# Performance work log

Measured on AMD Instinct MI355X. Metric: run time of the kernel, lower is better.

Reference implementation:

```python
import jax, jax.numpy as jnp
import numpy as np

N_NODES = 100000
N_EDGES = 300000
D_NODE_IN = 128
D_EDGE_IN = 4
LATENT = 256
HIDDEN = 256
STEPS = 6
D_OUT = 128
LN_EPS = 1e-5


def _mlp(x, w1, b1, w2, b2):
    # hk.nets.MLP([HIDDEN, out], activation=swish): act on hidden, none on output
    return jax.nn.swish(x @ w1 + b1) @ w2 + b2


def _ln(x, scale, offset):
    m = jnp.mean(x, axis=-1, keepdims=True)
    c = x - m
    v = jnp.mean(c * c, axis=-1, keepdims=True)
    return c * jax.lax.rsqrt(v + LN_EPS) * scale + offset


def setup_inputs():
    key = jax.random.key(0)
    ks = iter(jax.random.split(key, 40))

    def w(shape):
        fan_in = shape[-2]
        return (jax.random.normal(next(ks), shape, jnp.float32) / np.sqrt(fan_in).astype(np.float32))

    inp = {}
    inp['node_features'] = jax.random.normal(next(ks), (N_NODES, D_NODE_IN), jnp.float32)
    inp['edge_features'] = jax.random.normal(next(ks), (N_EDGES, D_EDGE_IN), jnp.float32)
    inp['senders'] = jax.random.randint(next(ks), (N_EDGES,), 0, N_NODES, jnp.int32)
    inp['receivers'] = jax.random.randint(next(ks), (N_EDGES,), 0, N_NODES, jnp.int32)
    # encoder (embed) MLPs + LayerNorm
    inp['enc_node_w1'] = w((D_NODE_IN, HIDDEN)); inp['enc_node_b1'] = jnp.zeros((HIDDEN,), jnp.float32)
    inp['enc_node_w2'] = w((HIDDEN, LATENT)); inp['enc_node_b2'] = jnp.zeros((LATENT,), jnp.float32)
    inp['enc_node_ln_s'] = jnp.ones((LATENT,), jnp.float32); inp['enc_node_ln_o'] = jnp.zeros((LATENT,), jnp.float32)
    inp['enc_edge_w1'] = w((D_EDGE_IN, HIDDEN)); inp['enc_edge_b1'] = jnp.zeros((HIDDEN,), jnp.float32)
    inp['enc_edge_w2'] = w((HIDDEN, LATENT)); inp['enc_edge_b2'] = jnp.zeros((LATENT,), jnp.float32)
    inp['enc_edge_ln_s'] = jnp.ones((LATENT,), jnp.float32); inp['enc_edge_ln_o'] = jnp.zeros((LATENT,), jnp.float32)
    # processor: STEPS unshared InteractionNetwork layers, weights stacked on axis 0
    inp['pe_w1'] = w((STEPS, 3 * LATENT, HIDDEN)); inp['pe_b1'] = jnp.zeros((STEPS, HIDDEN), jnp.float32)
    inp['pe_w2'] = w((STEPS, HIDDEN, LATENT)); inp['pe_b2'] = jnp.zeros((STEPS, LATENT), jnp.float32)
    inp['pe_ln_s'] = jnp.ones((STEPS, LATENT), jnp.float32); inp['pe_ln_o'] = jnp.zeros((STEPS, LATENT), jnp.float32)
    inp['pn_w1'] = w((STEPS, 2 * LATENT, HIDDEN)); inp['pn_b1'] = jnp.zeros((STEPS, HIDDEN), jnp.float32)
    inp['pn_w2'] = w((STEPS, HIDDEN, LATENT)); inp['pn_b2'] = jnp.zeros((STEPS, LATENT), jnp.float32)
    inp['pn_ln_s'] = jnp.ones((STEPS, LATENT), jnp.float32); inp['pn_ln_o'] = jnp.zeros((STEPS, LATENT), jnp.float32)
    # decoder (output) MLP, no LayerNorm
    inp['dec_w1'] = w((LATENT, HIDDEN)); inp['dec_b1'] = jnp.zeros((HIDDEN,), jnp.float32)
    inp['dec_w2'] = w((HIDDEN, D_OUT)); inp['dec_b2'] = jnp.zeros((D_OUT,), jnp.float32)
    return inp


def reference(node_features, edge_features, senders, receivers,
              enc_node_w1, enc_node_b1, enc_node_w2, enc_node_b2, enc_node_ln_s, enc_node_ln_o,
              enc_edge_w1, enc_edge_b1, enc_edge_w2, enc_edge_b2, enc_edge_ln_s, enc_edge_ln_o,
              pe_w1, pe_b1, pe_w2, pe_b2, pe_ln_s, pe_ln_o,
              pn_w1, pn_b1, pn_w2, pn_b2, pn_ln_s, pn_ln_o,
              dec_w1, dec_b1, dec_w2, dec_b2):
    # Embed nodes and edges into latent space (MLP + LayerNorm).
    node = _ln(_mlp(node_features, enc_node_w1, enc_node_b1, enc_node_w2, enc_node_b2), enc_node_ln_s, enc_node_ln_o)
    edge = _ln(_mlp(edge_features, enc_edge_w1, enc_edge_b1, enc_edge_w2, enc_edge_b2), enc_edge_ln_s, enc_edge_ln_o)

    n_nodes = node.shape[0]

    def step(carry, p):
        node, edge = carry
        ew1, eb1, ew2, eb2, els, elo, nw1, nb1, nw2, nb2, nls, nlo = p
        # edge update: MLP(concat[edge, sender_node, receiver_node]) + residual
        msg_in = jnp.concatenate([edge, node[senders], node[receivers]], axis=-1)  # [E, 3*LATENT]
        edge = edge + _ln(_mlp(msg_in, ew1, eb1, ew2, eb2), els, elo)
        # aggregate messages to receiver nodes
        agg = jax.ops.segment_sum(edge, receivers, num_segments=n_nodes)  # [N, LATENT]
        # node update: MLP(concat[node, agg]) + residual
        node = node + _ln(_mlp(jnp.concatenate([node, agg], axis=-1), nw1, nb1, nw2, nb2), nls, nlo)
        return (node, edge), None

    (node, edge), _ = jax.lax.scan(
        step, (node, edge),
        (pe_w1, pe_b1, pe_w2, pe_b2, pe_ln_s, pe_ln_o,
         pn_w1, pn_b1, pn_w2, pn_b2, pn_ln_s, pn_ln_o))

    # decoder: plain MLP (no LayerNorm) on nodes only (node_output_size given).
    return _mlp(node, dec_w1, dec_b1, dec_w2, dec_b2)  # [N, D_OUT]
```

## Files before the change

### kernel.cpp

```cpp
#include <hip/hip_runtime.h>
#include <hip/hip_bf16.h>


#define NN 100000
#define NE 300000

typedef __attribute__((ext_vector_type(8))) short bf16x8;
typedef __attribute__((ext_vector_type(8))) unsigned short u16x8;
typedef __attribute__((ext_vector_type(4))) float f32x4;

typedef const __attribute__((address_space(1))) void cg1_t;
typedef __attribute__((address_space(3))) void l3_t;
static __device__ __forceinline__ void gld_lds16(const void* g, void* l) {
  __builtin_amdgcn_global_load_lds((cg1_t*)g, (l3_t*)l, 16, 0, 0);
}

static __device__ __forceinline__ unsigned short f2bf(float f) {
  union { float f; unsigned u; } v; v.f = f;
  unsigned r = v.u + 0x7FFFu + ((v.u >> 16) & 1u);
  unsigned short h = (unsigned short)(r >> 16);
  if ((h & 0x7F80u) == 0x7F80u) h = 0;
  return h;
}
static __device__ __forceinline__ float bf2f(unsigned short h) {
  union { unsigned u; float f; } v; v.u = ((unsigned)h) << 16;
  return v.f;
}

struct KArgs {
  const float* Xf;
  unsigned short* nodeB;
  unsigned short* edgeB;
  const unsigned short* aggB;
  const int* snd;
  const int* rcv;
  const unsigned short* W1p;
  const unsigned short* W2p;
  const float* b1;
  const float* b2;
  const float* lns;
  const float* lno;
  float* outF;
  int M;
};

__global__ void pack_w(const float* __restrict__ src,
                       unsigned short* __restrict__ dst,
                       int Ksrc, int Kpad, int N) {
  src += (size_t)blockIdx.y * Ksrc * N;
  dst += (size_t)blockIdx.y * Kpad * N;
  int fi = blockIdx.x;
  int nfr = N >> 4;
  int nb = fi % nfr, kb = fi / nfr;
  int t = threadIdx.x;
  int lane = t >> 3, j = t & 7;
  int k = kb * 32 + ((lane >> 4) * 8) + j;
  int col = nb * 16 + (lane & 15);
  unsigned short v = (k < Ksrc) ? f2bf(src[(size_t)k * N + col]) : (unsigned short)0;
  dst[(size_t)fi * 512 + t] = v;
}

__global__ void zero_ws(uint4* __restrict__ p, int n16) {
  uint4 z = {0u, 0u, 0u, 0u};
  for (int i = blockIdx.x * blockDim.x + threadIdx.x; i < n16;
       i += gridDim.x * blockDim.x)
    p[i] = z;
}

__global__ void hist_k(const int* __restrict__ rcv, int* __restrict__ cnt) {
  int e = blockIdx.x * blockDim.x + threadIdx.x;
  if (e < NE) {
    int r = rcv[e]; r = r < 0 ? 0 : (r > NN - 1 ? NN - 1 : r);
    atomicAdd(&cnt[r], 1);
  }
}

__global__ __launch_bounds__(1024)
void scan_k(const int* __restrict__ cnt, int* __restrict__ off) {
  __shared__ int wsum[16];
  __shared__ int carry_s, tot_s;
  int t = threadIdx.x, lane = t & 63, w = t >> 6;
  if (t == 0) carry_s = 0;
  __syncthreads();
  for (int base = 0; base < NN; base += 1024) {
    int i = base + t;
    int v = (i < NN) ? cnt[i] : 0;
    int incl = v;
    #pragma unroll
    for (int d = 1; d < 64; d <<= 1) {
      int u = __shfl_up(incl, d);
      if (lane >= d) incl += u;
    }
    if (lane == 63) wsum[w] = incl;
    int c0 = carry_s;
    __syncthreads();
    if (t < 16) {
      int s = wsum[t];
      int isc = s;
      #pragma unroll
      for (int d = 1; d < 16; d <<= 1) {
        int u = __shfl_up(isc, d);
        if (t >= d) isc += u;
      }
      wsum[t] = isc - s;
    }
    __syncthreads();
    int excl = c0 + wsum[w] + incl - v;
    if (i < NN) off[i] = excl;
    if (t == 1023) tot_s = wsum[15] + incl;
    __syncthreads();
    if (t == 0) carry_s += tot_s;
    __syncthreads();
  }
  if (t == 0) off[NN] = carry_s;
}

__global__ void fill_k(const int* __restrict__ rcv, const int* __restrict__ off,
                       int* __restrict__ cnt2, int* __restrict__ eidx) {
  int e = blockIdx.x * blockDim.x + threadIdx.x;
  if (e < NE) {
    int r = rcv[e]; r = r < 0 ? 0 : (r > NN - 1 ? NN - 1 : r);
    int p = off[r] + atomicAdd(&cnt2[r], 1);
    if (p >= 0 && p < NE) eidx[p] = e;
  }
}

__global__ __launch_bounds__(256)
void agg_k(const unsigned short* __restrict__ edge, const int* __restrict__ off,
           const int* __restrict__ eidx, unsigned short* __restrict__ agg) {
  int t = threadIdx.x;
  int n0 = blockIdx.x * 8;
  #pragma unroll 1
  for (int u = 0; u < 8; ++u) {
    int n = n0 + u;
    if (n >= NN) return;
    int s = off[n], e = off[n + 1];
    if (s < 0) s = 0;
    if (e > NE) e = NE;
    float acc = 0.f;
    for (int i = s; i < e; ++i) {
      int eid = eidx[i];
      eid = eid < 0 ? 0 : (eid > NE - 1 ? NE - 1 : eid);
      acc += bf2f(edge[(size_t)eid * 256 + t]);
    }
    agg[(size_t)n * 256 + t] = f2bf(acc);
  }
}

template<int PHASE>
__global__ __launch_bounds__(512)
void gnn_kernel(KArgs A) {
  constexpr int K1  = PHASE==0?128 : PHASE==1?64 : PHASE==2?768 : PHASE==3?512 : 256;
  constexpr int NS1 = K1 / 64;
  constexpr int N2  = (PHASE==4) ? 128 : 256;
  constexpr int NF2 = N2 / 128;

  __shared__ __align__(16) char smem[50688];
  auto Ht  = (unsigned short (*)[264])(smem + 16384);
  int*   lidx = (int*)(smem + 50176);
  float* ps    = (float*)smem;
  float* ps2   = (float*)(smem + 2048);
  float* rs_mu = (float*)(smem + 4096);
  float* rs_rs = (float*)(smem + 4352);

  const int tid  = threadIdx.x;
  const int wid  = tid >> 6;
  const int lane = tid & 63;
  const int r0   = blockIdx.x * 64;
  const int M    = A.M;

  if constexpr (PHASE == 2) {
    if (tid < 64) {
      int e = r0 + tid; if (e > M - 1) e = M - 1;
      int v = A.snd[e]; v = v < 0 ? 0 : (v > NN - 1 ? NN - 1 : v);
      lidx[tid] = v;
    } else if (tid < 128) {
      int e = r0 + tid - 64; if (e > M - 1) e = M - 1;
      int v = A.rcv[e]; v = v < 0 ? 0 : (v > NN - 1 ? NN - 1 : v);
      lidx[tid] = v;
    }
  }
  __syncthreads();

  auto stage = [&](int ks, int b) {
    int r = tid >> 3;
    int c = (tid & 7) ^ (r & 7);
    int row = r0 + r; if (row > M - 1) row = M - 1;
    if constexpr (PHASE == 0) {
      const float* s = A.Xf + (size_t)row * 128 + ks * 64 + c * 8;
      float4 f0 = *(const float4*)s;
      float4 f1 = *(const float4*)(s + 4);
      u16x8 w;
      w[0]=f2bf(f0.x); w[1]=f2bf(f0.y); w[2]=f2bf(f0.z); w[3]=f2bf(f0.w);
      w[4]=f2bf(f1.x); w[5]=f2bf(f1.y); w[6]=f2bf(f1.z); w[7]=f2bf(f1.w);
      *(u16x8*)(smem + b * 8192 + r * 128 + (tid & 7) * 16) = w;
    } else if constexpr (PHASE == 1) {
      u16x8 w = (u16x8){0,0,0,0,0,0,0,0};
      if (c == 0) {
        float4 f = *(const float4*)(A.Xf + (size_t)row * 4);
        w[0]=f2bf(f.x); w[1]=f2bf(f.y); w[2]=f2bf(f.z); w[3]=f2bf(f.w);
      }
      *(u16x8*)(smem + b * 8192 + r * 128 + (tid & 7) * 16) = w;
    } else {
      const unsigned short* src;
      if constexpr (PHASE == 2) {
        if (ks < 4) {
          src = A.edgeB + (size_t)row * 256 + ks * 64 + c * 8;
        } else {
          int nidx = (ks < 8) ? lidx[r] : lidx[64 + r];
          int koff = (ks < 8) ? (ks - 4) * 64 : (ks - 8) * 64;
          src = A.nodeB + (size_t)nidx * 256 + koff + c * 8;
        }
      } else if constexpr (PHASE == 3) {
        src = (ks < 4) ? A.nodeB + (size_t)row * 256 + ks * 64 + c * 8
                       : A.aggB  + (size_t)row * 256 + (ks - 4) * 64 + c * 8;
      } else {
        src = A.nodeB + (size_t)row * 256 + ks * 64 + c * 8;
      }
      gld_lds16(src, smem + b * 8192 + wid * 1024);
    }
  };

  const int mrow  = lane & 15;
  const int rbase = (lane >> 4) * 4;
  const int swz   = mrow & 7;

  f32x4 zero4 = {0.f, 0.f, 0.f, 0.f};
  f32x4 acc1[4][2];
  #pragma unroll
  for (int m = 0; m < 4; ++m) { acc1[m][0] = zero4; acc1[m][1] = zero4; }

  stage(0, 0);
  __syncthreads();
  for (int ks = 0; ks < NS1; ++ks) {
    if (ks + 1 < NS1) stage(ks + 1, (ks + 1) & 1);
    const char* buf = smem + (ks & 1) * 8192;
    #pragma unroll
    for (int kk = 0; kk < 2; ++kk) {
      int ch = (kk * 4 + (lane >> 4)) ^ swz;
      const char* p0 = buf + (mrow) * 128 + ch * 16;
      bf16x8 a0 = *(const bf16x8*)(p0);
      bf16x8 a1 = *(const bf16x8*)(p0 + 16 * 128);
      bf16x8 a2 = *(const bf16x8*)(p0 + 32 * 128);
      bf16x8 a3 = *(const bf16x8*)(p0 + 48 * 128);
      bf16x8 b0 = *(const bf16x8*)(A.W1p + ((size_t)((2 * ks + kk) * 16 + wid * 2 + 0) * 64 + lane) * 8);
      bf16x8 b1 = *(const bf16x8*)(A.W1p + ((size_t)((2 * ks + kk) * 16 + wid * 2 + 1) * 64 + lane) * 8);
      acc1[0][0] = __builtin_amdgcn_mfma_f32_16x16x32_bf16(a0, b0, acc1[0][0], 0, 0, 0);
      acc1[0][1] = __builtin_amdgcn_mfma_f32_16x16x32_bf16(a0, b1, acc1[0][1], 0, 0, 0);
      acc1[1][0] = __builtin_amdgcn_mfma_f32_16x16x32_bf16(a1, b0, acc1[1][0], 0, 0, 0);
      acc1[1][1] = __builtin_amdgcn_mfma_f32_16x16x32_bf16(a1, b1, acc1[1][1], 0, 0, 0);
      acc1[2][0] = __builtin_amdgcn_mfma_f32_16x16x32_bf16(a2, b0, acc1[2][0], 0, 0, 0);
      acc1[2][1] = __builtin_amdgcn_mfma_f32_16x16x32_bf16(a2, b1, acc1[2][1], 0, 0, 0);
      acc1[3][0] = __builtin_amdgcn_mfma_f32_16x16x32_bf16(a3, b0, acc1[3][0], 0, 0, 0);
      acc1[3][1] = __builtin_amdgcn_mfma_f32_16x16x32_bf16(a3, b1, acc1[3][1], 0, 0, 0);
    }
    __syncthreads();
  }

  #pragma unroll
  for (int nf = 0; nf < 2; ++nf) {
    int c = wid * 32 + nf * 16 + mrow;
    float bb = A.b1[c];
    #pragma unroll
    for (int m = 0; m < 4; ++m)
      #pragma unroll
      for (int j = 0; j < 4; ++j) {
        float x = acc1[m][nf][j] + bb;
        float h = x * (1.f / (1.f + __expf(-x)));
        Ht[m * 16 + rbase + j][c] = f2bf(h);
      }
  }
  __syncthreads();

  f32x4 acc2[4][NF2];
  #pragma unroll
  for (int m = 0; m < 4; ++m)
    #pragma unroll
    for (int nf = 0; nf < NF2; ++nf) acc2[m][nf] = zero4;

  const int kof = (lane >> 4) * 8;
  #pragma unroll
  for (int ks = 0; ks < 8; ++ks) {
    bf16x8 a[4], b[NF2];
    #pragma unroll
    for (int m = 0; m < 4; ++m)
      a[m] = *(const bf16x8*)&Ht[m * 16 + mrow][ks * 32 + kof];
    #pragma unroll
    for (int nf = 0; nf < NF2; ++nf)
      b[nf] = *(const bf16x8*)(A.W2p + ((size_t)(ks * (N2 / 16) + wid * NF2 + nf) * 64 + lane) * 8);
    #pragma unroll
    for (int m = 0; m < 4; ++m)
      #pragma unroll
      for (int nf = 0; nf < NF2; ++nf)
        acc2[m][nf] = __builtin_amdgcn_mfma_f32_16x16x32_bf16(a[m], b[nf], acc2[m][nf], 0, 0, 0);
  }

  if constexpr (PHASE == 4) {
    int c = wid * 16 + mrow;
    float bb = A.b2[c];
    #pragma unroll
    for (int m = 0; m < 4; ++m)
      #pragma unroll
      for (int j = 0; j < 4; ++j) {
        int rg = r0 + m * 16 + rbase + j;
        if (rg < M) A.outF[(size_t)rg * 128 + c] = acc2[m][0][j] + bb;
      }
  } else {
    const int cc0 = wid * 32 + mrow;
    const int cc1 = cc0 + 16;
    const float bb0 = A.b2[cc0];
    const float bb1 = A.b2[cc1];
    #pragma unroll
    for (int m = 0; m < 4; ++m)
      #pragma unroll
      for (int j = 0; j < 4; ++j) {
        acc2[m][0][j] += bb0;
        acc2[m][1][j] += bb1;
        float t  = acc2[m][0][j] + acc2[m][1][j];
        float t2 = acc2[m][0][j] * acc2[m][0][j] + acc2[m][1][j] * acc2[m][1][j];
        #pragma unroll
        for (int mk = 1; mk < 16; mk <<= 1) {
          t  += __shfl_xor(t, mk);
          t2 += __shfl_xor(t2, mk);
        }
        if (mrow == 0) {
          int row = m * 16 + rbase + j;
          ps [wid * 64 + row] = t;
          ps2[wid * 64 + row] = t2;
        }
      }
    __syncthreads();
    if (tid < 64) {
      float s = 0.f, q = 0.f;
      #pragma unroll
      for (int w = 0; w < 8; ++w) { s += ps[w * 64 + tid]; q += ps2[w * 64 + tid]; }
      float mu = s * (1.0f / 256.0f);
      float va = fmaxf(q * (1.0f / 256.0f) - mu * mu, 0.f);
      rs_mu[tid] = mu;
      rs_rs[tid] = rsqrtf(va + 1e-5f);
    }
    __syncthreads();
    const float ls0 = A.lns[cc0], lo0 = A.lno[cc0];
    const float ls1 = A.lns[cc1], lo1 = A.lno[cc1];
    #pragma unroll
    for (int m = 0; m < 4; ++m)
      #pragma unroll
      for (int j = 0; j < 4; ++j) {
        int row = m * 16 + rbase + j;
        int rg = r0 + row;
        if (rg >= M) continue;
        float mu = rs_mu[row], rstd = rs_rs[row];
        float y0 = (acc2[m][0][j] - mu) * rstd * ls0 + lo0;
        float y1 = (acc2[m][1][j] - mu) * rstd * ls1 + lo1;
        size_t base = (size_t)rg * 256;
        if constexpr (PHASE == 0) {
          A.nodeB[base + cc0] = f2bf(y0);
          A.nodeB[base + cc1] = f2bf(y1);
        } else if constexpr (PHASE == 1) {
          A.edgeB[base + cc0] = f2bf(y0);
          A.edgeB[base + cc1] = f2bf(y1);
        } else if constexpr (PHASE == 2) {
          A.edgeB[base + cc0] = f2bf(bf2f(A.edgeB[base + cc0]) + y0);
          A.edgeB[base + cc1] = f2bf(bf2f(A.edgeB[base + cc1]) + y1);
        } else {
          A.nodeB[base + cc0] = f2bf(bf2f(A.nodeB[base + cc0]) + y0);
          A.nodeB[base + cc1] = f2bf(bf2f(A.nodeB[base + cc1]) + y1);
        }
      }
  }
}

extern "C" void kernel_launch(void* const* d_in, const int* in_sizes, int n_in,
                              void* d_out, int out_size, void* d_ws, size_t ws_size,
                              hipStream_t stream) {
  (void)in_sizes; (void)n_in; (void)out_size; (void)ws_size;
  const float* x_node = (const float*)d_in[0];
  const float* x_edge = (const float*)d_in[1];
  const int* snd = (const int*)d_in[2];
  const int* rcv = (const int*)d_in[3];
  const float* en_w1 = (const float*)d_in[4];
  const float* en_b1 = (const float*)d_in[5];
  const float* en_w2 = (const float*)d_in[6];
  const float* en_b2 = (const float*)d_in[7];
  const float* en_ls = (const float*)d_in[8];
  const float* en_lo = (const float*)d_in[9];
  const float* ee_w1 = (const float*)d_in[10];
  const float* ee_b1 = (const float*)d_in[11];
  const float* ee_w2 = (const float*)d_in[12];
  const float* ee_b2 = (const float*)d_in[13];
  const float* ee_ls = (const float*)d_in[14];
  const float* ee_lo = (const float*)d_in[15];
  const float* pe_w1 = (const float*)d_in[16];
  const float* pe_b1 = (const float*)d_in[17];
  const float* pe_w2 = (const float*)d_in[18];
  const float* pe_b2 = (const float*)d_in[19];
  const float* pe_ls = (const float*)d_in[20];
  const float* pe_lo = (const float*)d_in[21];
  const float* pn_w1 = (const float*)d_in[22];
  const float* pn_b1 = (const float*)d_in[23];
  const float* pn_w2 = (const float*)d_in[24];
  const float* pn_b2 = (const float*)d_in[25];
  const float* pn_ls = (const float*)d_in[26];
  const float* pn_lo = (const float*)d_in[27];
  const float* dc_w1 = (const float*)d_in[28];
  const float* dc_b1 = (const float*)d_in[29];
  const float* dc_w2 = (const float*)d_in[30];
  const float* dc_b2 = (const float*)d_in[31];

  char* ws = (char*)d_ws;
  unsigned short* edgeB = (unsigned short*)(ws);
  unsigned short* nodeB = (unsigned short*)(ws + 153600000LL);
  unsigned short* aggB  = (unsigned short*)(ws + 204800000LL);

  unsigned short* wpck = (unsigned short*)d_out;
  size_t o = 0;
  auto nxt = [&](size_t n) { unsigned short* p = wpck + o; o += n; return p; };
  unsigned short* p_en_w1 = nxt(128 * 256);
  unsigned short* p_en_w2 = nxt(256 * 256);
  unsigned short* p_ee_w1 = nxt(64 * 256);
  unsigned short* p_ee_w2 = nxt(256 * 256);
  unsigned short* p_pe_w1 = nxt((size_t)6 * 768 * 256);
  unsigned short* p_pe_w2 = nxt((size_t)6 * 256 * 256);
  unsigned short* p_pn_w1 = nxt((size_t)6 * 512 * 256);
  unsigned short* p_pn_w2 = nxt((size_t)6 * 256 * 256);
  unsigned short* p_dc_w1 = nxt(256 * 256);
  unsigned short* p_dc_w2 = nxt(256 * 128);
  const size_t DC_BYTES = (256 * 256 + 256 * 128) * 2;

  char* outc = (char*)d_out;
  int* cnt  = (int*)(outc + 6062080);
  int* cnt2 = (int*)(outc + 6462080);
  int* off  = (int*)(outc + 6862080);
  int* eidx = (int*)(outc + 7262096);

  dim3 B(512);
  pack_w<<<dim3(4 * 16, 1), B, 0, stream>>>(en_w1, p_en_w1, 128, 128, 256);
  pack_w<<<dim3(8 * 16, 1), B, 0, stream>>>(en_w2, p_en_w2, 256, 256, 256);
  pack_w<<<dim3(2 * 16, 1), B, 0, stream>>>(ee_w1, p_ee_w1, 4, 64, 256);
  pack_w<<<dim3(8 * 16, 1), B, 0, stream>>>(ee_w2, p_ee_w2, 256, 256, 256);
  pack_w<<<dim3(24 * 16, 6), B, 0, stream>>>(pe_w1, p_pe_w1, 768, 768, 256);
  pack_w<<<dim3(8 * 16, 6), B, 0, stream>>>(pe_w2, p_pe_w2, 256, 256, 256);
  pack_w<<<dim3(16 * 16, 6), B, 0, stream>>>(pn_w1, p_pn_w1, 512, 512, 256);
  pack_w<<<dim3(8 * 16, 6), B, 0, stream>>>(pn_w2, p_pn_w2, 256, 256, 256);
  pack_w<<<dim3(8 * 16, 1), B, 0, stream>>>(dc_w1, p_dc_w1, 256, 256, 256);
  pack_w<<<dim3(8 * 8, 1), B, 0, stream>>>(dc_w2, p_dc_w2, 256, 256, 128);

  zero_ws<<<dim3(196), dim3(256), 0, stream>>>((uint4*)cnt, 800000 / 16);
  hist_k<<<dim3(1172), dim3(256), 0, stream>>>(rcv, cnt);
  scan_k<<<dim3(1), dim3(1024), 0, stream>>>(cnt, off);
  fill_k<<<dim3(1172), dim3(256), 0, stream>>>(rcv, off, cnt2, eidx);

  dim3 GN(1563), GE(4688);

  {
    KArgs a{}; a.Xf = x_node; a.W1p = p_en_w1; a.W2p = p_en_w2;
    a.b1 = en_b1; a.b2 = en_b2; a.lns = en_ls; a.lno = en_lo;
    a.nodeB = nodeB; a.M = NN;
    gnn_kernel<0><<<GN, B, 0, stream>>>(a);
  }
  {
    KArgs a{}; a.Xf = x_edge; a.W1p = p_ee_w1; a.W2p = p_ee_w2;
    a.b1 = ee_b1; a.b2 = ee_b2; a.lns = ee_ls; a.lno = ee_lo;
    a.edgeB = edgeB; a.M = NE;
    gnn_kernel<1><<<GE, B, 0, stream>>>(a);
  }
  for (int s = 0; s < 6; ++s) {
    {
      KArgs a{}; a.snd = snd; a.rcv = rcv;
      a.nodeB = nodeB; a.edgeB = edgeB;
      a.W1p = p_pe_w1 + (size_t)s * 768 * 256;
      a.W2p = p_pe_w2 + (size_t)s * 256 * 256;
      a.b1 = pe_b1 + s * 256; a.b2 = pe_b2 + s * 256;
      a.lns = pe_ls + s * 256; a.lno = pe_lo + s * 256;
      a.M = NE;
      gnn_kernel<2><<<GE, B, 0, stream>>>(a);
    }
    agg_k<<<dim3(12500), dim3(256), 0, stream>>>(edgeB, off, eidx, aggB);
    {
      KArgs a{}; a.nodeB = nodeB; a.aggB = aggB;
      a.W1p = p_pn_w1 + (size_t)s * 512 * 256;
      a.W2p = p_pn_w2 + (size_t)s * 256 * 256;
      a.b1 = pn_b1 + s * 256; a.b2 = pn_b2 + s * 256;
      a.lns = pn_ls + s * 256; a.lno = pn_lo + s * 256;
      a.M = NN;
      gnn_kernel<3><<<GN, B, 0, stream>>>(a);
    }
  }
  hipMemcpyAsync((void*)aggB, p_dc_w1, DC_BYTES, hipMemcpyDeviceToDevice, stream);
  {
    KArgs a{}; a.nodeB = nodeB;
    a.W1p = (const unsigned short*)aggB;
    a.W2p = (const unsigned short*)aggB + 256 * 256;
    a.b1 = dc_b1; a.b2 = dc_b2;
    a.outF = (float*)d_out; a.M = NN;
    gnn_kernel<4><<<GN, B, 0, stream>>>(a);
  }
}
```

Before: 3.191 ms.

## Deepen global-to-LDS prefetch and register-prefetch weights in GEMM1 K-loop

For the bf16 input phases, the first-GEMM K-loop now keeps two global_load_lds stages in flight. It waits with explicit vmcnt counts and raw s_barrier instead of __syncthreads, so the gather loads for the next tile overlap the current MFMAs. Weight fragments for the next K-step are loaded into registers one iteration ahead. Precomputed source pointers remove per-stage index arithmetic. The manual waitcnt handling is fragile: the register weight loads also count toward vmcnt, which may make the waits over-conservative or ordering-sensitive, and the prefetch raises register pressure.

```diff
diff --git a/kernel.cpp b/kernel.cpp
--- a/kernel.cpp
+++ b/kernel.cpp
@@ -182,45 +182,6 @@
   }
   __syncthreads();
 
-  auto stage = [&](int ks, int b) {
-    int r = tid >> 3;
-    int c = (tid & 7) ^ (r & 7);
-    int row = r0 + r; if (row > M - 1) row = M - 1;
-    if constexpr (PHASE == 0) {
-      const float* s = A.Xf + (size_t)row * 128 + ks * 64 + c * 8;
-      float4 f0 = *(const float4*)s;
-      float4 f1 = *(const float4*)(s + 4);
-      u16x8 w;
-      w[0]=f2bf(f0.x); w[1]=f2bf(f0.y); w[2]=f2bf(f0.z); w[3]=f2bf(f0.w);
-      w[4]=f2bf(f1.x); w[5]=f2bf(f1.y); w[6]=f2bf(f1.z); w[7]=f2bf(f1.w);
-      *(u16x8*)(smem + b * 8192 + r * 128 + (tid & 7) * 16) = w;
-    } else if constexpr (PHASE == 1) {
-      u16x8 w = (u16x8){0,0,0,0,0,0,0,0};
-      if (c == 0) {
-        float4 f = *(const float4*)(A.Xf + (size_t)row * 4);
-        w[0]=f2bf(f.x); w[1]=f2bf(f.y); w[2]=f2bf(f.z); w[3]=f2bf(f.w);
-      }
-      *(u16x8*)(smem + b * 8192 + r * 128 + (tid & 7) * 16) = w;
-    } else {
-      const unsigned short* src;
-      if constexpr (PHASE == 2) {
-        if (ks < 4) {
-          src = A.edgeB + (size_t)row * 256 + ks * 64 + c * 8;
-        } else {
-          int nidx = (ks < 8) ? lidx[r] : lidx[64 + r];
-          int koff = (ks < 8) ? (ks - 4) * 64 : (ks - 8) * 64;
-          src = A.nodeB + (size_t)nidx * 256 + koff + c * 8;
-        }
-      } else if constexpr (PHASE == 3) {
-        src = (ks < 4) ? A.nodeB + (size_t)row * 256 + ks * 64 + c * 8
-                       : A.aggB  + (size_t)row * 256 + (ks - 4) * 64 + c * 8;
-      } else {
-        src = A.nodeB + (size_t)row * 256 + ks * 64 + c * 8;
-      }
-      gld_lds16(src, smem + b * 8192 + wid * 1024);
-    }
-  };
-
   const int mrow  = lane & 15;
   const int rbase = (lane >> 4) * 4;
   const int swz   = mrow & 7;
@@ -230,31 +191,126 @@
   #pragma unroll
   for (int m = 0; m < 4; ++m) { acc1[m][0] = zero4; acc1[m][1] = zero4; }
 
-  stage(0, 0);
-  __syncthreads();
-  for (int ks = 0; ks < NS1; ++ks) {
-    if (ks + 1 < NS1) stage(ks + 1, (ks + 1) & 1);
-    const char* buf = smem + (ks & 1) * 8192;
-    #pragma unroll
-    for (int kk = 0; kk < 2; ++kk) {
-      int ch = (kk * 4 + (lane >> 4)) ^ swz;
-      const char* p0 = buf + (mrow) * 128 + ch * 16;
-      bf16x8 a0 = *(const bf16x8*)(p0);
-      bf16x8 a1 = *(const bf16x8*)(p0 + 16 * 128);
-      bf16x8 a2 = *(const bf16x8*)(p0 + 32 * 128);
-      bf16x8 a3 = *(const bf16x8*)(p0 + 48 * 128);
-      bf16x8 b0 = *(const bf16x8*)(A.W1p + ((size_t)((2 * ks + kk) * 16 + wid * 2 + 0) * 64 + lane) * 8);
-      bf16x8 b1 = *(const bf16x8*)(A.W1p + ((size_t)((2 * ks + kk) * 16 + wid * 2 + 1) * 64 + lane) * 8);
-      acc1[0][0] = __builtin_amdgcn_mfma_f32_16x16x32_bf16(a0, b0, acc1[0][0], 0, 0, 0);
-      acc1[0][1] = __builtin_amdgcn_mfma_f32_16x16x32_bf16(a0, b1, acc1[0][1], 0, 0, 0);
-      acc1[1][0] = __builtin_amdgcn_mfma_f32_16x16x32_bf16(a1, b0, acc1[1][0], 0, 0, 0);
-      acc1[1][1] = __builtin_amdgcn_mfma_f32_16x16x32_bf16(a1, b1, acc1[1][1], 0, 0, 0);
-      acc1[2][0] = __builtin_amdgcn_mfma_f32_16x16x32_bf16(a2, b0, acc1[2][0], 0, 0, 0);
-      acc1[2][1] = __builtin_amdgcn_mfma_f32_16x16x32_bf16(a2, b1, acc1[2][1], 0, 0, 0);
-      acc1[3][0] = __builtin_amdgcn_mfma_f32_16x16x32_bf16(a3, b0, acc1[3][0], 0, 0, 0);
-      acc1[3][1] = __builtin_amdgcn_mfma_f32_16x16x32_bf16(a3, b1, acc1[3][1], 0, 0, 0);
-    }
-    __syncthreads();
+  if constexpr (PHASE <= 1) {
+    auto stage = [&](int ks, int b) {
+      int r = tid >> 3;
+      int c = (tid & 7) ^ (r & 7);
+      int row = r0 + r; if (row > M - 1) row = M - 1;
+      u16x8 w;
+      if constexpr (PHASE == 0) {
+        const float* s = A.Xf + (size_t)row * 128 + ks * 64 + c * 8;
+        float4 f0 = *(const float4*)s;
+        float4 f1 = *(const float4*)(s + 4);
+        w[0]=f2bf(f0.x); w[1]=f2bf(f0.y); w[2]=f2bf(f0.z); w[3]=f2bf(f0.w);
+        w[4]=f2bf(f1.x); w[5]=f2bf(f1.y); w[6]=f2bf(f1.z); w[7]=f2bf(f1.w);
+      } else {
+        w = (u16x8){0,0,0,0,0,0,0,0};
+        if (c == 0) {
+          float4 f = *(const float4*)(A.Xf + (size_t)row * 4);
+          w[0]=f2bf(f.x); w[1]=f2bf(f.y); w[2]=f2bf(f.z); w[3]=f2bf(f.w);
+        }
+      }
+      *(u16x8*)(smem + b * 8192 + (tid >> 3) * 128 + (tid & 7) * 16) = w;
+    };
+    stage(0, 0);
+    __syncthreads();
+    #pragma unroll
+    for (int ks = 0; ks < NS1; ++ks) {
+      if (ks + 1 < NS1) stage(ks + 1, (ks + 1) & 1);
+      const char* buf = smem + (ks & 1) * 8192;
+      #pragma unroll
+      for (int kk = 0; kk < 2; ++kk) {
+        int ch = (kk * 4 + (lane >> 4)) ^ swz;
+        const char* p0 = buf + mrow * 128 + ch * 16;
+        bf16x8 a0 = *(const bf16x8*)(p0);
+        bf16x8 a1 = *(const bf16x8*)(p0 + 16 * 128);
+        bf16x8 a2 = *(const bf16x8*)(p0 + 32 * 128);
+        bf16x8 a3 = *(const bf16x8*)(p0 + 48 * 128);
+        const unsigned short* wb = A.W1p + ((size_t)((2 * ks + kk) * 16 + wid * 2) * 64 + lane) * 8;
+        bf16x8 b0 = *(const bf16x8*)(wb);
+        bf16x8 b1 = *(const bf16x8*)(wb + 512);
+        acc1[0][0] = __builtin_amdgcn_mfma_f32_16x16x32_bf16(a0, b0, acc1[0][0], 0, 0, 0);
+        acc1[0][1] = __builtin_amdgcn_mfma_f32_16x16x32_bf16(a0, b1, acc1[0][1], 0, 0, 0);
+        acc1[1][0] = __builtin_amdgcn_mfma_f32_16x16x32_bf16(a1, b0, acc1[1][0], 0, 0, 0);
+        acc1[1][1] = __builtin_amdgcn_mfma_f32_16x16x32_bf16(a1, b1, acc1[1][1], 0, 0, 0);
+        acc1[2][0] = __builtin_amdgcn_mfma_f32_16x16x32_bf16(a2, b0, acc1[2][0], 0, 0, 0);
+        acc1[2][1] = __builtin_amdgcn_mfma_f32_16x16x32_bf16(a2, b1, acc1[2][1], 0, 0, 0);
+        acc1[3][0] = __builtin_amdgcn_mfma_f32_16x16x32_bf16(a3, b0, acc1[3][0], 0, 0, 0);
+        acc1[3][1] = __builtin_amdgcn_mfma_f32_16x16x32_bf16(a3, b1, acc1[3][1], 0, 0, 0);
+      }
+      __syncthreads();
+    }
+  } else {
+    int r = tid >> 3;
+    int cs = ((tid & 7) ^ (r & 7)) * 8;
+    int row = r0 + r; if (row > M - 1) row = M - 1;
+    const unsigned short *s0 = nullptr, *s1 = nullptr, *s2 = nullptr;
+    if constexpr (PHASE == 2) {
+      s0 = A.edgeB + (size_t)row * 256 + cs;
+      s1 = A.nodeB + (size_t)lidx[r] * 256 + cs;
+      s2 = A.nodeB + (size_t)lidx[64 + r] * 256 + cs;
+    } else if constexpr (PHASE == 3) {
+      s0 = A.nodeB + (size_t)row * 256 + cs;
+      s1 = A.aggB + (size_t)row * 256 + cs;
+    } else {
+      s0 = A.nodeB + (size_t)row * 256 + cs;
+    }
+    auto issue = [&](int ks, int b) {
+      const unsigned short* src;
+      if constexpr (PHASE == 2)
+        src = ks < 4 ? s0 + ks * 64 : (ks < 8 ? s1 + (ks - 4) * 64 : s2 + (ks - 8) * 64);
+      else if constexpr (PHASE == 3)
+        src = ks < 4 ? s0 + ks * 64 : s1 + (ks - 4) * 64;
+      else
+        src = s0 + ks * 64;
+      gld_lds16(src, smem + b * 8192 + wid * 1024);
+    };
+    const unsigned short* w1base = A.W1p + ((size_t)(wid * 2) * 64 + lane) * 8;
+    auto load_b = [&](int ks, bf16x8* bk0, bf16x8* bk1) {
+      const unsigned short* wb0 = w1base + (size_t)(2 * ks) * 16 * 512;
+      const unsigned short* wb1 = w1base + (size_t)(2 * ks + 1) * 16 * 512;
+      bk0[0] = *(const bf16x8*)(wb0); bk0[1] = *(const bf16x8*)(wb0 + 512);
+      bk1[0] = *(const bf16x8*)(wb1); bk1[1] = *(const bf16x8*)(wb1 + 512);
+    };
+
+    issue(0, 0);
+    issue(1, 1);
+    bf16x8 c0[2], c1[2], n0[2], n1[2];
+    load_b(0, c0, c1);
+    #pragma unroll
+    for (int ks = 0; ks < NS1; ++ks) {
+      if (ks < NS1 - 1) asm volatile("s_waitcnt vmcnt(1)" ::: "memory");
+      else              asm volatile("s_waitcnt vmcnt(0)" ::: "memory");
+      __builtin_amdgcn_sched_barrier(0);
+      __builtin_amdgcn_s_barrier();
+      __builtin_amdgcn_sched_barrier(0);
+      if (ks + 1 < NS1) load_b(ks + 1, n0, n1);
+      const char* buf = smem + (ks & 1) * 8192;
+      #pragma unroll
+      for (int kk = 0; kk < 2; ++kk) {
+        int ch = (kk * 4 + (lane >> 4)) ^ swz;
+        const char* p0 = buf + mrow * 128 + ch * 16;
+        bf16x8 a0 = *(const bf16x8*)(p0);
+        bf16x8 a1 = *(const bf16x8*)(p0 + 16 * 128);
+        bf16x8 a2 = *(const bf16x8*)(p0 + 32 * 128);
+        bf16x8 a3 = *(const bf16x8*)(p0 + 48 * 128);
+        bf16x8 b0 = kk ? c1[0] : c0[0];
+        bf16x8 b1 = kk ? c1[1] : c0[1];
+        acc1[0][0] = __builtin_amdgcn_mfma_f32_16x16x32_bf16(a0, b0, acc1[0][0], 0, 0, 0);
+        acc1[0][1] = __builtin_amdgcn_mfma_f32_16x16x32_bf16(a0, b1, acc1[0][1], 0, 0, 0);
+        acc1[1][0] = __builtin_amdgcn_mfma_f32_16x16x32_bf16(a1, b0, acc1[1][0], 0, 0, 0);
+        acc1[1][1] = __builtin_amdgcn_mfma_f32_16x16x32_bf16(a1, b1, acc1[1][1], 0, 0, 0);
+        acc1[2][0] = __builtin_amdgcn_mfma_f32_16x16x32_bf16(a2, b0, acc1[2][0], 0, 0, 0);
+        acc1[2][1] = __builtin_amdgcn_mfma_f32_16x16x32_bf16(a2, b1, acc1[2][1], 0, 0, 0);
+        acc1[3][0] = __builtin_amdgcn_mfma_f32_16x16x32_bf16(a3, b0, acc1[3][0], 0, 0, 0);
+        acc1[3][1] = __builtin_amdgcn_mfma_f32_16x16x32_bf16(a3, b1, acc1[3][1], 0, 0, 0);
+      }
+      __builtin_amdgcn_sched_barrier(0);
+      __builtin_amdgcn_s_barrier();
+      __builtin_amdgcn_sched_barrier(0);
+      if (ks + 2 < NS1) issue(ks + 2, ks & 1);
+      c0[0] = n0[0]; c0[1] = n0[1]; c1[0] = n1[0]; c1[1] = n1[1];
+    }
   }
 
   #pragma unroll
```

Result: faster. 2.713 ms (median of 2 runs) (-15.0%).
